# Kernel tuning notes

Measured on AMD Instinct MI355X. Metric: run time of the kernel, lower is better.

The kernel has to match this reference:

```python
import jax, jax.numpy as jnp
import numpy as np
import math

B, S, D, H = 4, 2048, 1024, 16
DH = D // H


def _make_random_mask(key, seq_length):
    # Vectorized equivalent of create_random_mask: keep exactly seq_length//2
    # uniformly-random positions per row.
    scores = jax.random.uniform(key, (seq_length, seq_length))
    kth = jax.lax.top_k(scores, seq_length // 2)[0][:, -1:]  # per-row threshold
    return scores >= kth  # bool [S, S], exactly S//2 True per row


def setup_inputs() -> dict:
    key = jax.random.key(0)
    ks = jax.random.split(key, 10)
    s = 1.0 / math.sqrt(D)
    return {
        "hidden_states": jax.random.normal(ks[0], (B, S, D), jnp.float32),
        "mask": _make_random_mask(ks[1], S),
        "Wq": jax.random.normal(ks[2], (D, D), jnp.float32) * s,
        "bq": jnp.zeros((D,), jnp.float32),
        "Wk": jax.random.normal(ks[3], (D, D), jnp.float32) * s,
        "bk": jnp.zeros((D,), jnp.float32),
        "Wv": jax.random.normal(ks[4], (D, D), jnp.float32) * s,
        "bv": jnp.zeros((D,), jnp.float32),
        "Wo": jax.random.normal(ks[5], (D, D), jnp.float32) * s,
        "bo": jnp.zeros((D,), jnp.float32),
    }


def reference(hidden_states, mask, Wq, bq, Wk, bk, Wv, bv, Wo, bo):
    b, s, d = hidden_states.shape
    scale = 1.0 / math.sqrt(DH)

    def heads(x):  # [B,S,D] -> [B,H,S,DH]
        return x.reshape(b, s, H, DH).transpose(0, 2, 1, 3)

    q = heads(hidden_states @ Wq + bq)
    k = heads(hidden_states @ Wk + bk)
    v = heads(hidden_states @ Wv + bv)

    scores = jnp.einsum("bhqd,bhkd->bhqk", q, k) * scale
    scores = jnp.where(mask[None, None], scores, jnp.float32(-1e9))
    probs = jax.nn.softmax(scores, axis=-1)  # attn_dropout rate = 0 (eval)

    ctx = jnp.einsum("bhqk,bhkd->bhqd", probs, v)
    ctx = ctx.transpose(0, 2, 1, 3).reshape(b, s, d)
    return ctx @ Wo + bo  # proj_dropout rate = 0 (eval); vis=False -> weights None
```

## Files before the change

kernel.cpp:

```cpp
#include <hip/hip_runtime.h>

typedef unsigned short u16;
typedef unsigned int   u32;
typedef unsigned long long u64;
typedef unsigned char  u8;
typedef __attribute__((ext_vector_type(8))) short bf16x8;
typedef __attribute__((ext_vector_type(4))) float f32x4;

#define B_  4
#define S_  2048
#define D_  1024
#define H_  16
#define DH_ 64
#define M_  (B_*S_)

__device__ __forceinline__ u16 f2bf(float f) {
  u32 u = __builtin_bit_cast(u32, f);
  u32 r = (u + 0x7FFFu + ((u >> 16) & 1u)) >> 16;
  return (u16)r;
}

__device__ __forceinline__ void gload_lds16(const void* g, void* l) {
  __builtin_amdgcn_global_load_lds(
      (const __attribute__((address_space(1))) u32*)g,
      (__attribute__((address_space(3))) u32*)l,
      16, 0, 0);
}

__device__ __forceinline__ bf16x8 lds_frag(const u16* base, int row, int cb) {
  return *(const bf16x8*)((const char*)base + row * 128 + (cb ^ ((row & 7) << 4)));
}

__global__ __launch_bounds__(256) void convert_x(const float* __restrict__ x,
                                                 u16* __restrict__ xb) {
  const int i = (blockIdx.x * 256 + threadIdx.x) * 4;
  float4 v = *(const float4*)(x + i);
  ushort4 o;
  o.x = f2bf(v.x); o.y = f2bf(v.y); o.z = f2bf(v.z); o.w = f2bf(v.w);
  *(ushort4*)(xb + i) = o;
}

__global__ __launch_bounds__(256) void transpose_w(
    const float* __restrict__ W0, const float* __restrict__ W1,
    const float* __restrict__ W2, const float* __restrict__ W3,
    u16* __restrict__ T0, u16* __restrict__ T1,
    u16* __restrict__ T2, u16* __restrict__ T3) {
  __shared__ float t[64][65];
  const int z = blockIdx.z;
  const float* W = z == 0 ? W0 : z == 1 ? W1 : z == 2 ? W2 : W3;
  u16* T        = z == 0 ? T0 : z == 1 ? T1 : z == 2 ? T2 : T3;
  const int n0 = blockIdx.x * 64, k0 = blockIdx.y * 64;
  const int c = threadIdx.x & 63, r0 = threadIdx.x >> 6;
#pragma unroll
  for (int i = 0; i < 16; i++)
    t[r0 + i * 4][c] = W[(size_t)(k0 + r0 + i * 4) * 1024 + n0 + c];
  __syncthreads();
#pragma unroll
  for (int i = 0; i < 16; i++)
    T[(size_t)(n0 + r0 + i * 4) * 1024 + k0 + c] = f2bf(t[c][r0 + i * 4]);
}

__global__ __launch_bounds__(256) void pack_mask(const int* __restrict__ m,
                                                 u64* __restrict__ mb) {
  const int i = blockIdx.x * 256 + threadIdx.x;
  const u64 bits = __ballot(m[i] != 0);
  if ((threadIdx.x & 63) == 0) mb[i >> 6] = bits;
}

__global__ __launch_bounds__(256) void fuse_bias(const float* __restrict__ bq,
                                                 const float* __restrict__ bk,
                                                 const float* __restrict__ bv,
                                                 float* __restrict__ fb) {
  const int i = blockIdx.x * 256 + threadIdx.x;
  fb[i] = i < 1024 ? bq[i] : (i < 2048 ? bk[i - 1024] : bv[i - 2048]);
}

__global__ __launch_bounds__(256) void gemm_bt(
    const u16* __restrict__ A, const u16* __restrict__ Bw,
    const float* __restrict__ bias, void* __restrict__ outp, int mode) {
  __shared__ u16 As[128 * 32];
  __shared__ u16 Bs[128 * 32];
  const int tid = threadIdx.x;
  const int lane = tid & 63, wid = tid >> 6;
  const int wr = wid >> 1, wc = wid & 1;
  const int bm = blockIdx.x, bn = blockIdx.y;
  const int lr = lane & 15, lk8 = (lane >> 4) * 8, lg = (lane >> 4) * 4;

  f32x4 zero = {0.f, 0.f, 0.f, 0.f};
  f32x4 acc[4][4];
#pragma unroll
  for (int i = 0; i < 4; i++)
#pragma unroll
    for (int j = 0; j < 4; j++) acc[i][j] = zero;

  const int r0 = tid >> 2;
  const int c0 = (tid & 3) * 8;
  const u16* gA = A + ((size_t)(bm * 128 + r0) << 10) + c0;
  const u16* gB = Bw + ((size_t)(bn * 128 + r0) << 10) + c0;
  u16* lA = &As[tid * 8];
  u16* lB = &Bs[tid * 8];

  for (int kt = 0; kt < 1024; kt += 32) {
    gload_lds16(gA + kt, lA);
    gload_lds16(gA + kt + (64 << 10), lA + 64 * 32);
    gload_lds16(gB + kt, lB);
    gload_lds16(gB + kt + (64 << 10), lB + 64 * 32);
    __syncthreads();

    bf16x8 af[4], bfr[4];
#pragma unroll
    for (int mr = 0; mr < 4; mr++)
      af[mr] = *(const bf16x8*)&As[(wr * 64 + mr * 16 + lr) * 32 + lk8];
#pragma unroll
    for (int nr = 0; nr < 4; nr++)
      bfr[nr] = *(const bf16x8*)&Bs[(wc * 64 + nr * 16 + lr) * 32 + lk8];
#pragma unroll
    for (int mr = 0; mr < 4; mr++)
#pragma unroll
      for (int nr = 0; nr < 4; nr++)
        acc[mr][nr] = __builtin_amdgcn_mfma_f32_16x16x32_bf16(af[mr], bfr[nr],
                                                              acc[mr][nr], 0, 0, 0);
    __syncthreads();
  }

#pragma unroll
  for (int mr = 0; mr < 4; mr++) {
#pragma unroll
    for (int nr = 0; nr < 4; nr++) {
      const int n = bn * 128 + wc * 64 + nr * 16 + lr;
      const float bv = bias[n];
#pragma unroll
      for (int r = 0; r < 4; r++) {
        const int m = bm * 128 + wr * 64 + mr * 16 + lg + r;
        float v = acc[mr][nr][r] + bv;
        if (mode == 2) {
          ((float*)outp)[(size_t)m * 1024 + n] = v;
        } else {
          const int which = n >> 10, col = n & 1023;
          const int bb = m >> 11, s = m & (S_ - 1);
          const int hh = col >> 6, dh = col & (DH_ - 1);
          if (which == 0) v *= 0.125f;
          u16* o = (u16*)outp + ((size_t)which << 23);
          if (which <= 1)
            o[((((size_t)bb * H_ + hh) * S_ + s) << 6) + dh] = f2bf(v);
          else
            o[(((size_t)(bb * H_ + hh) * DH_ + dh) << 11) + s] = f2bf(v);
        }
      }
    }
  }
}

__global__ __launch_bounds__(256) void attn(
    const u16* __restrict__ Q, const u16* __restrict__ K,
    const u16* __restrict__ Vt, const u64* __restrict__ mb,
    u16* __restrict__ ctx) {
  __shared__ u16 Kl[64 * 64];
  __shared__ u16 Vl[64 * 64];
  __shared__ u16 Pl[4][16 * 64];

  const int tid = threadIdx.x, lane = tid & 63, wid = tid >> 6;
  const int q0 = blockIdx.x * 64;
  const int h = blockIdx.y, b = blockIdx.z;
  const size_t bh = (size_t)b * H_ + h;
  const u16* Qb = Q + (bh * S_ << 6);
  const u16* Kb = K + (bh * S_ << 6);
  const u16* Vb = Vt + (bh * DH_ << 11);
  const int lr = lane & 15, g = lane >> 4, lk8 = g * 8, lg = g * 4;

  const bf16x8 qf0 = *(const bf16x8*)(Qb + ((size_t)(q0 + wid * 16 + lr) << 6) + lk8);
  const bf16x8 qf1 = *(const bf16x8*)(Qb + ((size_t)(q0 + wid * 16 + lr) << 6) + 32 + lk8);

  f32x4 zero = {0.f, 0.f, 0.f, 0.f};
  f32x4 acc[4];
#pragma unroll
  for (int i = 0; i < 4; i++) acc[i] = zero;
  float mrow[4] = {-1e30f, -1e30f, -1e30f, -1e30f};
  float lrow[4] = {0.f, 0.f, 0.f, 0.f};

  const int sr = tid >> 3;
  const int scz = ((((tid & 7) * 16) ^ ((sr & 7) << 4)) >> 1);
  u16* lK = &Kl[tid * 8];
  u16* lV = &Vl[tid * 8];
  const int qrow_base = q0 + wid * 16 + lg;

  for (int kt = 0; kt < S_; kt += 64) {
    u64 mw[4];
#pragma unroll
    for (int r = 0; r < 4; r++)
      mw[r] = mb[(size_t)(qrow_base + r) * 32 + (kt >> 6)];

    gload_lds16(Kb + ((size_t)(kt + sr) << 6) + scz, lK);
    gload_lds16(Kb + ((size_t)(kt + sr + 32) << 6) + scz, lK + 32 * 64);
    gload_lds16(Vb + ((size_t)sr << 11) + kt + scz, lV);
    gload_lds16(Vb + ((size_t)(sr + 32) << 11) + kt + scz, lV + 32 * 64);
    __syncthreads();

    f32x4 sc4[4];
    __builtin_amdgcn_s_setprio(1);
#pragma unroll
    for (int nr = 0; nr < 4; nr++) {
      const int row = nr * 16 + lr;
      const bf16x8 kf0 = lds_frag(Kl, row, lk8 * 2);
      const bf16x8 kf1 = lds_frag(Kl, row, 64 + lk8 * 2);
      f32x4 z = zero;
      z = __builtin_amdgcn_mfma_f32_16x16x32_bf16(qf0, kf0, z, 0, 0, 0);
      z = __builtin_amdgcn_mfma_f32_16x16x32_bf16(qf1, kf1, z, 0, 0, 0);
      sc4[nr] = z;
    }
    __builtin_amdgcn_s_setprio(0);

#pragma unroll
    for (int nr = 0; nr < 4; nr++)
#pragma unroll
      for (int r = 0; r < 4; r++)
        if (!((mw[r] >> (nr * 16 + lr)) & 1ull)) sc4[nr][r] = -1e9f;

#pragma unroll
    for (int r = 0; r < 4; r++) {
      float mx = fmaxf(fmaxf(sc4[0][r], sc4[1][r]), fmaxf(sc4[2][r], sc4[3][r]));
      mx = fmaxf(mx, __shfl_xor(mx, 1));
      mx = fmaxf(mx, __shfl_xor(mx, 2));
      mx = fmaxf(mx, __shfl_xor(mx, 4));
      mx = fmaxf(mx, __shfl_xor(mx, 8));
      const float mnew = fmaxf(mrow[r], mx);
      const float alpha = __expf(mrow[r] - mnew);
      mrow[r] = mnew;
      float ps = 0.f;
#pragma unroll
      for (int nr = 0; nr < 4; nr++) {
        const float p = __expf(sc4[nr][r] - mnew);
        sc4[nr][r] = p;
        ps += p;
      }
      ps += __shfl_xor(ps, 1);
      ps += __shfl_xor(ps, 2);
      ps += __shfl_xor(ps, 4);
      ps += __shfl_xor(ps, 8);
      lrow[r] = lrow[r] * alpha + ps;
#pragma unroll
      for (int nc = 0; nc < 4; nc++) acc[nc][r] *= alpha;
    }

    {
      char* pw = (char*)Pl[wid];
#pragma unroll
      for (int nr = 0; nr < 4; nr++)
#pragma unroll
        for (int r = 0; r < 4; r++) {
          const int qr = lg + r, cb = (nr * 16 + lr) * 2;
          *(u16*)(pw + qr * 128 + (cb ^ ((qr & 7) << 4))) = f2bf(sc4[nr][r]);
        }
    }

#pragma unroll
    for (int ks = 0; ks < 2; ks++) {
      const bf16x8 pf = lds_frag(Pl[wid], lr, ks * 64 + lk8 * 2);
      __builtin_amdgcn_s_setprio(1);
#pragma unroll
      for (int nc = 0; nc < 4; nc++) {
        const bf16x8 vf = lds_frag(Vl, nc * 16 + lr, ks * 64 + lk8 * 2);
        acc[nc] = __builtin_amdgcn_mfma_f32_16x16x32_bf16(pf, vf, acc[nc], 0, 0, 0);
      }
      __builtin_amdgcn_s_setprio(0);
    }
    __syncthreads();
  }

#pragma unroll
  for (int nc = 0; nc < 4; nc++)
#pragma unroll
    for (int r = 0; r < 4; r++) {
      const float o = acc[nc][r] / lrow[r];
      const int ql = q0 + wid * 16 + lg + r;
      ctx[((size_t)b * S_ + ql) * D_ + h * DH_ + nc * 16 + lr] = f2bf(o);
    }
}

extern "C" void kernel_launch(void* const* d_in, const int* in_sizes, int n_in,
                              void* d_out, int out_size, void* d_ws, size_t ws_size,
                              hipStream_t stream) {
  const float* X  = (const float*)d_in[0];
  const int* mask = (const int*)d_in[1];
  const float* Wq = (const float*)d_in[2];
  const float* bq = (const float*)d_in[3];
  const float* Wk = (const float*)d_in[4];
  const float* bk = (const float*)d_in[5];
  const float* Wv = (const float*)d_in[6];
  const float* bv = (const float*)d_in[7];
  const float* Wo = (const float*)d_in[8];
  const float* bo = (const float*)d_in[9];

  char* ws = (char*)d_ws;
  const size_t MB = 1024 * 1024;
  u16* xb  = (u16*)(ws);
  u16* q   = (u16*)(ws + 16 * MB);
  u16* wqt = (u16*)(ws + 64 * MB);
  u16* wkt = (u16*)(ws + 66 * MB);
  u16* wvt = (u16*)(ws + 68 * MB);
  u16* wot = (u16*)(ws + 70 * MB);
  u64* mbb = (u64*)(ws + 72 * MB);
  float* fb = (float*)(ws + 72 * MB + 512 * 1024);

  convert_x<<<8192, 256, 0, stream>>>(X, xb);
  transpose_w<<<dim3(16, 16, 4), 256, 0, stream>>>(Wq, Wk, Wv, Wo, wqt, wkt, wvt, wot);
  pack_mask<<<16384, 256, 0, stream>>>(mask, mbb);
  fuse_bias<<<12, 256, 0, stream>>>(bq, bk, bv, fb);

  gemm_bt<<<dim3(64, 24), 256, 0, stream>>>(xb, wqt, fb, q, 3);

  u16* k  = q + (1u << 23);
  u16* vt = q + (2u << 23);
  attn<<<dim3(S_ / 64, H_, B_), 256, 0, stream>>>(q, k, vt, mbb, xb);

  gemm_bt<<<dim3(64, 8), 256, 0, stream>>>(xb, wot, bo, d_out, 2);
}
```

Measured before the change: 442.1 us.

## Double-buffer GEMM and attention tiles, transpose softmax layout, fuse prep kernels

Fuses x conversion, mask packing and bias concat into one prep kernel. Adds double-buffered LDS staging in both the GEMM and the attention kernel so the next tile's global loads overlap compute. The attention kernel swaps the QK^T MFMA operands so each lane owns one query row, folds log2(e) into the Q scale so it can use raw exp2, skips the rescale when the running max grows by at most 8, and packs P with v_cvt_pk_bf16. LDS use doubles and the lazy rescale relies on a bounded exponent growth.

```diff
diff --git a/kernel.cpp b/kernel.cpp
--- a/kernel.cpp
+++ b/kernel.cpp
@@ -12,12 +12,25 @@
 #define D_  1024
 #define H_  16
 #define DH_ 64
-#define M_  (B_*S_)
+
+#define MFMA16 __builtin_amdgcn_mfma_f32_16x16x32_bf16
 
 __device__ __forceinline__ u16 f2bf(float f) {
   u32 u = __builtin_bit_cast(u32, f);
   u32 r = (u + 0x7FFFu + ((u >> 16) & 1u)) >> 16;
   return (u16)r;
+}
+
+__device__ __forceinline__ u32 cvt_pk_bf16(float lo, float hi) {
+  u32 r;
+  asm("v_cvt_pk_bf16_f32 %0, %1, %2" : "=v"(r) : "v"(lo), "v"(hi));
+  return r;
+}
+
+__device__ __forceinline__ float exp2_fast(float x) {
+  float r;
+  asm("v_exp_f32 %0, %1" : "=v"(r) : "v"(x));
+  return r;
 }
 
 __device__ __forceinline__ void gload_lds16(const void* g, void* l) {
@@ -31,13 +44,30 @@
   return *(const bf16x8*)((const char*)base + row * 128 + (cb ^ ((row & 7) << 4)));
 }
 
-__global__ __launch_bounds__(256) void convert_x(const float* __restrict__ x,
-                                                 u16* __restrict__ xb) {
-  const int i = (blockIdx.x * 256 + threadIdx.x) * 4;
-  float4 v = *(const float4*)(x + i);
-  ushort4 o;
-  o.x = f2bf(v.x); o.y = f2bf(v.y); o.z = f2bf(v.z); o.w = f2bf(v.w);
-  *(ushort4*)(xb + i) = o;
+__global__ __launch_bounds__(256) void prep(
+    const float* __restrict__ x, u16* __restrict__ xb,
+    const int* __restrict__ m, u64* __restrict__ mbw,
+    const float* __restrict__ bq, const float* __restrict__ bk,
+    const float* __restrict__ bv, float* __restrict__ fb) {
+  const int blk = blockIdx.x;
+  if (blk < 8192) {
+    const int i = (blk * 256 + threadIdx.x) * 4;
+    float4 v = *(const float4*)(x + i);
+    ushort4 o;
+    o.x = f2bf(v.x); o.y = f2bf(v.y); o.z = f2bf(v.z); o.w = f2bf(v.w);
+    *(ushort4*)(xb + i) = o;
+  } else if (blk < 8192 + 2048) {
+    const int base = (blk - 8192) * 2048;
+#pragma unroll
+    for (int it = 0; it < 8; it++) {
+      const int i = base + it * 256 + threadIdx.x;
+      const u64 bits = __ballot(m[i] != 0);
+      if ((threadIdx.x & 63) == 0) mbw[i >> 6] = bits;
+    }
+  } else {
+    const int i = (blk - 10240) * 256 + threadIdx.x;
+    fb[i] = i < 1024 ? bq[i] : (i < 2048 ? bk[i - 1024] : bv[i - 2048]);
+  }
 }
 
 __global__ __launch_bounds__(256) void transpose_w(
@@ -60,66 +90,57 @@
     T[(size_t)(n0 + r0 + i * 4) * 1024 + k0 + c] = f2bf(t[c][r0 + i * 4]);
 }
 
-__global__ __launch_bounds__(256) void pack_mask(const int* __restrict__ m,
-                                                 u64* __restrict__ mb) {
-  const int i = blockIdx.x * 256 + threadIdx.x;
-  const u64 bits = __ballot(m[i] != 0);
-  if ((threadIdx.x & 63) == 0) mb[i >> 6] = bits;
-}
-
-__global__ __launch_bounds__(256) void fuse_bias(const float* __restrict__ bq,
-                                                 const float* __restrict__ bk,
-                                                 const float* __restrict__ bv,
-                                                 float* __restrict__ fb) {
-  const int i = blockIdx.x * 256 + threadIdx.x;
-  fb[i] = i < 1024 ? bq[i] : (i < 2048 ? bk[i - 1024] : bv[i - 2048]);
-}
-
 __global__ __launch_bounds__(256) void gemm_bt(
     const u16* __restrict__ A, const u16* __restrict__ Bw,
     const float* __restrict__ bias, void* __restrict__ outp, int mode) {
-  __shared__ u16 As[128 * 32];
-  __shared__ u16 Bs[128 * 32];
+  __shared__ u16 As[2][128 * 32];
+  __shared__ u16 Bs[2][128 * 32];
   const int tid = threadIdx.x;
   const int lane = tid & 63, wid = tid >> 6;
   const int wr = wid >> 1, wc = wid & 1;
   const int bm = blockIdx.x, bn = blockIdx.y;
   const int lr = lane & 15, lk8 = (lane >> 4) * 8, lg = (lane >> 4) * 4;
 
-  f32x4 zero = {0.f, 0.f, 0.f, 0.f};
   f32x4 acc[4][4];
 #pragma unroll
   for (int i = 0; i < 4; i++)
 #pragma unroll
-    for (int j = 0; j < 4; j++) acc[i][j] = zero;
+    for (int j = 0; j < 4; j++) acc[i][j] = (f32x4){0.f, 0.f, 0.f, 0.f};
 
   const int r0 = tid >> 2;
   const int c0 = (tid & 3) * 8;
   const u16* gA = A + ((size_t)(bm * 128 + r0) << 10) + c0;
   const u16* gB = Bw + ((size_t)(bn * 128 + r0) << 10) + c0;
-  u16* lA = &As[tid * 8];
-  u16* lB = &Bs[tid * 8];
-
-  for (int kt = 0; kt < 1024; kt += 32) {
-    gload_lds16(gA + kt, lA);
-    gload_lds16(gA + kt + (64 << 10), lA + 64 * 32);
-    gload_lds16(gB + kt, lB);
-    gload_lds16(gB + kt + (64 << 10), lB + 64 * 32);
-    __syncthreads();
+
+#define GSTAGE(ki, bf) do {                                        \
+    const int kt_ = (ki) * 32;                                     \
+    gload_lds16(gA + kt_, &As[bf][tid * 8]);                       \
+    gload_lds16(gA + kt_ + (64 << 10), &As[bf][tid * 8 + 64 * 32]);\
+    gload_lds16(gB + kt_, &Bs[bf][tid * 8]);                       \
+    gload_lds16(gB + kt_ + (64 << 10), &Bs[bf][tid * 8 + 64 * 32]);\
+  } while (0)
+
+  GSTAGE(0, 0);
+  __syncthreads();
+
+  for (int ki = 0; ki < 32; ki++) {
+    const int cur = ki & 1;
+    if (ki + 1 < 32) GSTAGE(ki + 1, cur ^ 1);
 
     bf16x8 af[4], bfr[4];
 #pragma unroll
     for (int mr = 0; mr < 4; mr++)
-      af[mr] = *(const bf16x8*)&As[(wr * 64 + mr * 16 + lr) * 32 + lk8];
+      af[mr] = *(const bf16x8*)&As[cur][(wr * 64 + mr * 16 + lr) * 32 + lk8];
 #pragma unroll
     for (int nr = 0; nr < 4; nr++)
-      bfr[nr] = *(const bf16x8*)&Bs[(wc * 64 + nr * 16 + lr) * 32 + lk8];
+      bfr[nr] = *(const bf16x8*)&Bs[cur][(wc * 64 + nr * 16 + lr) * 32 + lk8];
+    __builtin_amdgcn_s_setprio(1);
 #pragma unroll
     for (int mr = 0; mr < 4; mr++)
 #pragma unroll
       for (int nr = 0; nr < 4; nr++)
-        acc[mr][nr] = __builtin_amdgcn_mfma_f32_16x16x32_bf16(af[mr], bfr[nr],
-                                                              acc[mr][nr], 0, 0, 0);
+        acc[mr][nr] = MFMA16(af[mr], bfr[nr], acc[mr][nr], 0, 0, 0);
+    __builtin_amdgcn_s_setprio(0);
     __syncthreads();
   }
 
@@ -139,7 +160,7 @@
           const int which = n >> 10, col = n & 1023;
           const int bb = m >> 11, s = m & (S_ - 1);
           const int hh = col >> 6, dh = col & (DH_ - 1);
-          if (which == 0) v *= 0.125f;
+          if (which == 0) v *= 0.180336880f;
           u16* o = (u16*)outp + ((size_t)which << 23);
           if (which <= 1)
             o[((((size_t)bb * H_ + hh) * S_ + s) << 6) + dh] = f2bf(v);
@@ -155,8 +176,8 @@
     const u16* __restrict__ Q, const u16* __restrict__ K,
     const u16* __restrict__ Vt, const u64* __restrict__ mb,
     u16* __restrict__ ctx) {
-  __shared__ u16 Kl[64 * 64];
-  __shared__ u16 Vl[64 * 64];
+  __shared__ u16 Kl[2][64 * 64];
+  __shared__ u16 Vl[2][64 * 64];
   __shared__ u16 Pl[4][16 * 64];
 
   const int tid = threadIdx.x, lane = tid & 63, wid = tid >> 6;
@@ -166,114 +187,133 @@
   const u16* Qb = Q + (bh * S_ << 6);
   const u16* Kb = K + (bh * S_ << 6);
   const u16* Vb = Vt + (bh * DH_ << 11);
-  const int lr = lane & 15, g = lane >> 4, lk8 = g * 8, lg = g * 4;
-
-  const bf16x8 qf0 = *(const bf16x8*)(Qb + ((size_t)(q0 + wid * 16 + lr) << 6) + lk8);
-  const bf16x8 qf1 = *(const bf16x8*)(Qb + ((size_t)(q0 + wid * 16 + lr) << 6) + 32 + lk8);
-
-  f32x4 zero = {0.f, 0.f, 0.f, 0.f};
+  const int qh = lane & 15, g = lane >> 4, lk8 = g * 8;
+  const int qrow = q0 + wid * 16 + qh;
+
+  const bf16x8 qf0 = *(const bf16x8*)(Qb + ((size_t)qrow << 6) + lk8);
+  const bf16x8 qf1 = *(const bf16x8*)(Qb + ((size_t)qrow << 6) + 32 + lk8);
+
   f32x4 acc[4];
 #pragma unroll
-  for (int i = 0; i < 4; i++) acc[i] = zero;
-  float mrow[4] = {-1e30f, -1e30f, -1e30f, -1e30f};
-  float lrow[4] = {0.f, 0.f, 0.f, 0.f};
+  for (int i = 0; i < 4; i++) acc[i] = (f32x4){0.f, 0.f, 0.f, 0.f};
+  float mrun = -1e30f, lrun = 0.f;
 
   const int sr = tid >> 3;
   const int scz = ((((tid & 7) * 16) ^ ((sr & 7) << 4)) >> 1);
-  u16* lK = &Kl[tid * 8];
-  u16* lV = &Vl[tid * 8];
-  const int qrow_base = q0 + wid * 16 + lg;
-
-  for (int kt = 0; kt < S_; kt += 64) {
-    u64 mw[4];
-#pragma unroll
-    for (int r = 0; r < 4; r++)
-      mw[r] = mb[(size_t)(qrow_base + r) * 32 + (kt >> 6)];
-
-    gload_lds16(Kb + ((size_t)(kt + sr) << 6) + scz, lK);
-    gload_lds16(Kb + ((size_t)(kt + sr + 32) << 6) + scz, lK + 32 * 64);
-    gload_lds16(Vb + ((size_t)sr << 11) + kt + scz, lV);
-    gload_lds16(Vb + ((size_t)(sr + 32) << 11) + kt + scz, lV + 32 * 64);
-    __syncthreads();
-
-    f32x4 sc4[4];
+
+#define ASTAGE(t, bf) do {                                                  \
+    const int kt_ = (t) * 64;                                               \
+    gload_lds16(Kb + ((size_t)(kt_ + sr) << 6) + scz, &Kl[bf][tid * 8]);    \
+    gload_lds16(Kb + ((size_t)(kt_ + sr + 32) << 6) + scz,                  \
+                &Kl[bf][tid * 8 + 32 * 64]);                                \
+    gload_lds16(Vb + ((size_t)sr << 11) + kt_ + scz, &Vl[bf][tid * 8]);     \
+    gload_lds16(Vb + ((size_t)(sr + 32) << 11) + kt_ + scz,                 \
+                &Vl[bf][tid * 8 + 32 * 64]);                                \
+  } while (0)
+
+  ASTAGE(0, 0);
+  __syncthreads();
+
+  for (int t = 0; t < S_ / 64; t++) {
+    const int cur = t & 1;
+    if (t + 1 < S_ / 64) ASTAGE(t + 1, cur ^ 1);
+    const u64 mw = mb[((size_t)qrow << 5) + t];
+
+    f32x4 sc[4];
     __builtin_amdgcn_s_setprio(1);
 #pragma unroll
     for (int nr = 0; nr < 4; nr++) {
-      const int row = nr * 16 + lr;
-      const bf16x8 kf0 = lds_frag(Kl, row, lk8 * 2);
-      const bf16x8 kf1 = lds_frag(Kl, row, 64 + lk8 * 2);
-      f32x4 z = zero;
-      z = __builtin_amdgcn_mfma_f32_16x16x32_bf16(qf0, kf0, z, 0, 0, 0);
-      z = __builtin_amdgcn_mfma_f32_16x16x32_bf16(qf1, kf1, z, 0, 0, 0);
-      sc4[nr] = z;
+      const int row = nr * 16 + qh;
+      const bf16x8 kf0 = lds_frag(Kl[cur], row, lk8 * 2);
+      const bf16x8 kf1 = lds_frag(Kl[cur], row, 64 + lk8 * 2);
+      f32x4 z = (f32x4){0.f, 0.f, 0.f, 0.f};
+      z = MFMA16(kf0, qf0, z, 0, 0, 0);
+      z = MFMA16(kf1, qf1, z, 0, 0, 0);
+      sc[nr] = z;
     }
     __builtin_amdgcn_s_setprio(0);
 
+    const u64 mwg = mw >> (g * 4);
+    const u32 mlo = (u32)mwg, mhi = (u32)(mwg >> 32);
+#pragma unroll
+    for (int nr = 0; nr < 4; nr++) {
+      const u32 wsel = (nr & 2) ? mhi : mlo;
+      const int sh = (nr & 1) * 16;
+#pragma unroll
+      for (int r = 0; r < 4; r++)
+        if (!((wsel >> (sh + r)) & 1u)) sc[nr][r] = -1e9f;
+    }
+
+    float tmax = sc[0][0];
 #pragma unroll
     for (int nr = 0; nr < 4; nr++)
 #pragma unroll
-      for (int r = 0; r < 4; r++)
-        if (!((mw[r] >> (nr * 16 + lr)) & 1ull)) sc4[nr][r] = -1e9f;
-
-#pragma unroll
-    for (int r = 0; r < 4; r++) {
-      float mx = fmaxf(fmaxf(sc4[0][r], sc4[1][r]), fmaxf(sc4[2][r], sc4[3][r]));
-      mx = fmaxf(mx, __shfl_xor(mx, 1));
-      mx = fmaxf(mx, __shfl_xor(mx, 2));
-      mx = fmaxf(mx, __shfl_xor(mx, 4));
-      mx = fmaxf(mx, __shfl_xor(mx, 8));
-      const float mnew = fmaxf(mrow[r], mx);
-      const float alpha = __expf(mrow[r] - mnew);
-      mrow[r] = mnew;
-      float ps = 0.f;
+      for (int r = 0; r < 4; r++) tmax = fmaxf(tmax, sc[nr][r]);
+    tmax = fmaxf(tmax, __shfl_xor(tmax, 16));
+    tmax = fmaxf(tmax, __shfl_xor(tmax, 32));
+
+    if (!__all(tmax <= mrun + 8.0f)) {
+      const float mnew = fmaxf(mrun, tmax);
+      const float alpha = exp2_fast(mrun - mnew);
+      lrun *= alpha;
+      mrun = mnew;
+#pragma unroll
+      for (int r = 0; r < 4; r++) {
+        const float as = __shfl(alpha, g * 4 + r);
+        acc[0][r] *= as; acc[1][r] *= as; acc[2][r] *= as; acc[3][r] *= as;
+      }
+    }
+
+    float ts = 0.f;
+    u32 w[8];
+#pragma unroll
+    for (int nr = 0; nr < 4; nr++) {
+      float p0 = exp2_fast(sc[nr][0] - mrun);
+      float p1 = exp2_fast(sc[nr][1] - mrun);
+      float p2 = exp2_fast(sc[nr][2] - mrun);
+      float p3 = exp2_fast(sc[nr][3] - mrun);
+      ts += (p0 + p1) + (p2 + p3);
+      w[nr * 2]     = cvt_pk_bf16(p0, p1);
+      w[nr * 2 + 1] = cvt_pk_bf16(p2, p3);
+    }
+    ts += __shfl_xor(ts, 16);
+    ts += __shfl_xor(ts, 32);
+    lrun += ts;
+
+    {
+      char* pw = (char*)Pl[wid] + qh * 128;
+      const int sw = (qh & 7) << 4;
 #pragma unroll
       for (int nr = 0; nr < 4; nr++) {
-        const float p = __expf(sc4[nr][r] - mnew);
-        sc4[nr][r] = p;
-        ps += p;
+        *(u32*)(pw + ((g * 8 + nr * 32) ^ sw))     = w[nr * 2];
+        *(u32*)(pw + ((g * 8 + 4 + nr * 32) ^ sw)) = w[nr * 2 + 1];
       }
-      ps += __shfl_xor(ps, 1);
-      ps += __shfl_xor(ps, 2);
-      ps += __shfl_xor(ps, 4);
-      ps += __shfl_xor(ps, 8);
-      lrow[r] = lrow[r] * alpha + ps;
-#pragma unroll
-      for (int nc = 0; nc < 4; nc++) acc[nc][r] *= alpha;
-    }
-
-    {
-      char* pw = (char*)Pl[wid];
-#pragma unroll
-      for (int nr = 0; nr < 4; nr++)
-#pragma unroll
-        for (int r = 0; r < 4; r++) {
-          const int qr = lg + r, cb = (nr * 16 + lr) * 2;
-          *(u16*)(pw + qr * 128 + (cb ^ ((qr & 7) << 4))) = f2bf(sc4[nr][r]);
-        }
     }
 
 #pragma unroll
     for (int ks = 0; ks < 2; ks++) {
-      const bf16x8 pf = lds_frag(Pl[wid], lr, ks * 64 + lk8 * 2);
+      const bf16x8 pf = lds_frag(Pl[wid], qh, ks * 64 + lk8 * 2);
       __builtin_amdgcn_s_setprio(1);
 #pragma unroll
       for (int nc = 0; nc < 4; nc++) {
-        const bf16x8 vf = lds_frag(Vl, nc * 16 + lr, ks * 64 + lk8 * 2);
-        acc[nc] = __builtin_amdgcn_mfma_f32_16x16x32_bf16(pf, vf, acc[nc], 0, 0, 0);
+        const bf16x8 vf = lds_frag(Vl[cur], nc * 16 + qh, ks * 64 + lk8 * 2);
+        acc[nc] = MFMA16(pf, vf, acc[nc], 0, 0, 0);
       }
       __builtin_amdgcn_s_setprio(0);
     }
     __syncthreads();
   }
 
+  float linv[4];
+#pragma unroll
+  for (int r = 0; r < 4; r++) linv[r] = 1.0f / __shfl(lrun, g * 4 + r);
 #pragma unroll
   for (int nc = 0; nc < 4; nc++)
 #pragma unroll
     for (int r = 0; r < 4; r++) {
-      const float o = acc[nc][r] / lrow[r];
-      const int ql = q0 + wid * 16 + lg + r;
-      ctx[((size_t)b * S_ + ql) * D_ + h * DH_ + nc * 16 + lr] = f2bf(o);
+      const float o = acc[nc][r] * linv[r];
+      const int ql = q0 + wid * 16 + g * 4 + r;
+      ctx[((size_t)b * S_ + ql) * D_ + h * DH_ + nc * 16 + qh] = f2bf(o);
     }
 }
 
@@ -302,10 +342,8 @@
   u64* mbb = (u64*)(ws + 72 * MB);
   float* fb = (float*)(ws + 72 * MB + 512 * 1024);
 
-  convert_x<<<8192, 256, 0, stream>>>(X, xb);
+  prep<<<10252, 256, 0, stream>>>(X, xb, mask, mbb, bq, bk, bv, fb);
   transpose_w<<<dim3(16, 16, 4), 256, 0, stream>>>(Wq, Wk, Wv, Wo, wqt, wkt, wvt, wot);
-  pack_mask<<<16384, 256, 0, stream>>>(mask, mbb);
-  fuse_bias<<<12, 256, 0, stream>>>(bq, bk, bv, fb);
 
   gemm_bt<<<dim3(64, 24), 256, 0, stream>>>(xb, wqt, fb, q, 3);
 
```

New measurement: 363.8 us. -17.7%, faster.
